# Optimization experiments

Hardware: AMD Instinct MI355X
Metric: run time of the kernel (lower is better)

Reference implementation:

```python
import jax, jax.numpy as jnp
import numpy as np

HEADS = 8
DIM_HEAD = 64
CHUNK = 128
EPS = 1e-6
KERNEL_EPS = 1e-4


def softmax_kernel(x, proj, is_query):
    # x: [b,h,n,d], proj: [f,d]  (FAVOR+ positive softmax features)
    d = x.shape[-1]
    data_normalizer = d ** -0.25
    ratio = proj.shape[0] ** -0.5
    data_dash = jnp.einsum('bhnd,fd->bhnf', x * data_normalizer, proj)
    diag = 0.5 * (data_normalizer ** 2) * jnp.sum(x * x, axis=-1, keepdims=True)  # [b,h,n,1]
    if is_query:
        m = jnp.max(data_dash, axis=-1, keepdims=True)
    else:
        m = jnp.max(data_dash, axis=(-1, -2), keepdims=True)
    return ratio * (jnp.exp(data_dash - diag - jax.lax.stop_gradient(m)) + KERNEL_EPS)


def infer_hidden_states(q, k, v, chunk_size=CHUNK):
    # q,k: [b,h,n,f], v: [b,h,n,e]; chunked causal linear attention with carried cumsums
    b, h, n, f = q.shape
    e = v.shape[-1]
    nc = n // chunk_size

    def to_chunks(t):
        return jnp.moveaxis(t.reshape(b, h, nc, chunk_size, t.shape[-1]), 2, 0)

    qs, ks, vs = to_chunks(q), to_chunks(k), to_chunks(v)

    def step(carry, inp):
        Z, S = carry  # [b,h,1,f], [b,h,1,f,e]
        qc, kc, vc = inp
        k_cum = Z + jnp.cumsum(kc, axis=2)                       # [b,h,c,f]
        D_inv = 1.0 / jnp.einsum('bhnf,bhnf->bhn', qc, k_cum + EPS)
        ctx = jnp.einsum('bhnf,bhne->bhnfe', kc, vc)             # [b,h,c,f,e]
        ctx_cum = S + jnp.cumsum(ctx, axis=2)
        out = jnp.einsum('bhnfe,bhnf,bhn->bhne', ctx_cum, qc, D_inv)
        return (k_cum[:, :, -1:], ctx_cum[:, :, -1:]), out

    init = (jnp.zeros((b, h, 1, f), q.dtype), jnp.zeros((b, h, 1, f, e), q.dtype))
    (Z, S), outs = jax.lax.scan(step, init, (qs, ks, vs))
    out = jnp.moveaxis(outs, 0, 2).reshape(b, h, n, e)
    return out, Z[:, :, 0], S[:, :, 0]


def reference(x, proj, Wq, Wk, Wv, Wo, bo):
    b, n, dim = x.shape
    h, dh = HEADS, DIM_HEAD

    def split_heads(t):
        return jnp.transpose(t.reshape(b, n, h, dh), (0, 2, 1, 3))

    q = split_heads(x @ Wq)
    k = split_heads(x @ Wk)
    v = split_heads(x @ Wv)

    qf = softmax_kernel(q, proj, is_query=True)
    kf = softmax_kernel(k, proj, is_query=False)

    out, Z, S = infer_hidden_states(qf, kf, v)
    out = jnp.transpose(out, (0, 2, 1, 3)).reshape(b, n, h * dh)
    out = out @ Wo + bo
    return out, Z, S


def setup_inputs() -> dict:
    key = jax.random.key(0)
    ks = jax.random.split(key, 6)
    b, n, dim = 2, 2048, 512
    f = 256
    return {
        'x': jax.random.normal(ks[0], (b, n, dim), jnp.float32),
        'proj': jax.random.normal(ks[1], (f, DIM_HEAD), jnp.float32),
        'Wq': jax.random.normal(ks[2], (dim, dim), jnp.float32) * (dim ** -0.5),
        'Wk': jax.random.normal(ks[3], (dim, dim), jnp.float32) * (dim ** -0.5),
        'Wv': jax.random.normal(ks[4], (dim, dim), jnp.float32) * (dim ** -0.5),
        'Wo': jax.random.normal(ks[5], (dim, dim), jnp.float32) * (dim ** -0.5),
        'bo': jnp.zeros((dim,), jnp.float32),
    }
```

## Files before the change

kernel.cpp:

```cpp
#include <hip/hip_runtime.h>
#include <hip/hip_bf16.h>
#include <math.h>

#define NB    2
#define NSEQ  2048
#define DIMM  512
#define NH    8
#define DHd   64
#define FF    256
#define CHK   128
#define NCHK  16
#define NBH   16

typedef unsigned short ushort_t;
typedef __attribute__((ext_vector_type(8))) __bf16 bf16x8;
typedef __attribute__((ext_vector_type(4))) float floatx4;

__device__ __forceinline__ unsigned short f2bf(float x) {
    union { __hip_bfloat16 h; unsigned short u; } v;
    v.h = __float2bfloat16(x);
    return v.u;
}
__device__ __forceinline__ float bf2f(unsigned short u) {
    union { unsigned short u2[2]; float f; } v;
    v.u2[0] = 0; v.u2[1] = u;
    return v.f;
}
__device__ __forceinline__ unsigned enc_f(float x) {
    unsigned u = __float_as_uint(x);
    return (u & 0x80000000u) ? ~u : (u | 0x80000000u);
}
__device__ __forceinline__ float dec_f(unsigned e) {
    unsigned u = (e & 0x80000000u) ? (e & 0x7fffffffu) : ~e;
    return __uint_as_float(u);
}

__device__ __forceinline__ void gload16(const void* g, void* l) {
    __builtin_amdgcn_global_load_lds(
        (const __attribute__((address_space(1))) void*)g,
        (__attribute__((address_space(3))) void*)l, 16, 0, 0);
}

__device__ __forceinline__ bf16x8 frag8(const ushort_t* lds, int row, int kb) {
    return *((const bf16x8*)lds + row * 8 + (kb ^ (row & 7)));
}
__device__ __forceinline__ bf16x8 fragS(const ushort_t* lds, int row, int kb) {
    return *((const bf16x8*)lds + row * 16 + (kb ^ (row & 15)));
}

__global__ __launch_bounds__(256)
void prep(const float* __restrict__ x, const float* __restrict__ proj,
          const float* __restrict__ W0, const float* __restrict__ W1,
          const float* __restrict__ W2, const float* __restrict__ W3,
          ushort_t* __restrict__ xb, ushort_t* __restrict__ projb,
          ushort_t* __restrict__ T0, ushort_t* __restrict__ T1,
          ushort_t* __restrict__ T2, ushort_t* __restrict__ T3,
          unsigned* __restrict__ mk_u)
{
    __shared__ float t[32][33];
    const int b = blockIdx.x, tid = threadIdx.x;
    if (b < 2048) {
        const int gid = b * 256 + tid;
        const float4 v = *(const float4*)(x + (size_t)gid * 4);
        union { ushort4 v4; unsigned short s[4]; } pk;
        pk.s[0] = f2bf(v.x); pk.s[1] = f2bf(v.y); pk.s[2] = f2bf(v.z); pk.s[3] = f2bf(v.w);
        ((ushort4*)xb)[gid] = pk.v4;
    } else if (b < 2064) {
        const int gid = (b - 2048) * 256 + tid;
        const float dn = 0.35355339059327379f;
        const float4 v = *(const float4*)(proj + (size_t)gid * 4);
        union { ushort4 v4; unsigned short s[4]; } pk;
        pk.s[0] = f2bf(v.x * dn); pk.s[1] = f2bf(v.y * dn);
        pk.s[2] = f2bf(v.z * dn); pk.s[3] = f2bf(v.w * dn);
        ((ushort4*)projb)[gid] = pk.v4;
    } else if (b < 3088) {
        const int idx = b - 2064;
        const int z = idx >> 8, rem = idx & 255;
        const int bx = rem & 15, by = rem >> 4;
        const float* W = (z == 0) ? W0 : (z == 1) ? W1 : (z == 2) ? W2 : W3;
        ushort_t* T = (z == 0) ? T0 : (z == 1) ? T1 : (z == 2) ? T2 : T3;
        const int x0 = bx * 32, y0 = by * 32;
        const int tx = tid & 31, ty = tid >> 5;
#pragma unroll
        for (int i = 0; i < 4; i++)
            t[ty + i * 8][tx] = W[(size_t)(y0 + ty + i * 8) * DIMM + x0 + tx];
        __syncthreads();
#pragma unroll
        for (int i = 0; i < 4; i++)
            T[(size_t)(x0 + ty + i * 8) * DIMM + y0 + tx] = f2bf(t[tx][ty + i * 8]);
    } else {
        if (tid < NBH) mk_u[tid] = 0u;
    }
}

__device__ __forceinline__ void mfma_mainloop(
    const ushort_t* __restrict__ AG, const ushort_t* __restrict__ BG,
    ushort_t* As, ushort_t* Bs, int ldA, int ldB, int K,
    floatx4 acc[4][4], int tid)
{
    const int lane = tid & 63, wid = tid >> 6;
    const int q = lane >> 4, c = lane & 15;
    const int wm = (wid >> 1) * 64, wn = (wid & 1) * 64;

    for (int k0 = 0; k0 < K; k0 += 64) {
#pragma unroll
        for (int t = 0; t < 4; t++) {
            const int g = t * 256 + tid, r = g >> 3, kb = (g & 7) ^ (r & 7);
            gload16(AG + (size_t)r * ldA + k0 + kb * 8, As + (size_t)g * 8);
        }
#pragma unroll
        for (int t = 0; t < 4; t++) {
            const int g = t * 256 + tid, r = g >> 3, kb = (g & 7) ^ (r & 7);
            gload16(BG + (size_t)r * ldB + k0 + kb * 8, Bs + (size_t)g * 8);
        }
        __syncthreads();
#pragma unroll
        for (int ks = 0; ks < 2; ks++) {
            bf16x8 af[4], bfr[4];
#pragma unroll
            for (int i = 0; i < 4; i++) {
                af[i]  = frag8(As, wm + i * 16 + c, ks * 4 + q);
                bfr[i] = frag8(Bs, wn + i * 16 + c, ks * 4 + q);
            }
#pragma unroll
            for (int i = 0; i < 4; i++)
#pragma unroll
                for (int j = 0; j < 4; j++)
                    acc[i][j] = __builtin_amdgcn_mfma_f32_16x16x32_bf16(
                        af[i], bfr[j], acc[i][j], 0, 0, 0);
        }
        __syncthreads();
    }
}

__global__ __launch_bounds__(256)
void gemm_qkv(const ushort_t* __restrict__ xb,
              const ushort_t* __restrict__ Wtq, const ushort_t* __restrict__ Wtk,
              const ushort_t* __restrict__ Wtv, const ushort_t* __restrict__ projb,
              ushort_t* __restrict__ qb, ushort_t* __restrict__ kb,
              ushort_t* __restrict__ vTb, unsigned* __restrict__ mk_u)
{
    __shared__ alignas(16) ushort_t SM[25600];
    __shared__ float red[256];
    ushort_t* As = SM;
    ushort_t* Bs = SM + 8192;
    ushort_t* PS = SM + 17408;
    const int tid = threadIdx.x;
    const int n0 = blockIdx.x * 128, m0 = blockIdx.y * 128, z = blockIdx.z;
    const ushort_t* Bt = (z == 0) ? Wtq : ((z == 1) ? Wtk : Wtv);

    floatx4 zero = {0.f, 0.f, 0.f, 0.f};
    floatx4 acc[4][4];
#pragma unroll
    for (int i = 0; i < 4; i++)
#pragma unroll
        for (int j = 0; j < 4; j++) acc[i][j] = zero;

    mfma_mainloop(xb + (size_t)m0 * DIMM, Bt + (size_t)n0 * DIMM, As, Bs,
                  DIMM, DIMM, DIMM, acc, tid);

    const int lane = tid & 63, wid = tid >> 6;
    const int q = lane >> 4, cl = lane & 15;
    const int wm = (wid >> 1) * 64, wn = (wid & 1) * 64;

#pragma unroll
    for (int i = 0; i < 4; i++)
#pragma unroll
        for (int j = 0; j < 4; j++) {
            const int col = wn + j * 16 + cl;
#pragma unroll
            for (int r = 0; r < 4; r++) {
                const int row = wm + i * 16 + q * 4 + r;
                SM[row * 136 + col] = f2bf(acc[i][j][r]);
            }
        }
    __syncthreads();

    if (z < 2) {
        ushort_t* ob = (z == 0) ? qb : kb;
        if (z == 1) {
#pragma unroll
            for (int t = 0; t < 4; t++) {
                const int g = t * 256 + tid, f = g >> 3, kbg = (g & 7) ^ (f & 7);
                gload16(projb + (size_t)f * 64 + kbg * 8, PS + (size_t)g * 8);
            }
        }
#pragma unroll
        for (int p = 0; p < 16; p++) {
            const int idx = p * 256 + tid;
            const int row = idx >> 5, c4 = idx & 31;
            ushort4 o = *(const ushort4*)&SM[row * 136 + c4 * 4];
            *(ushort4*)(ob + (size_t)(m0 + row) * DIMM + n0 + c4 * 4) = o;
        }
        if (z == 1) {
            const int bb = m0 >> 11;
            const int h0 = n0 >> 6;
            float mx[2] = {-3.0e38f, -3.0e38f};
#pragma unroll
            for (int half = 0; half < 2; half++) {
                __syncthreads();
#pragma unroll
                for (int hh = 0; hh < 2; hh++) {
                    floatx4 a2[4][4];
#pragma unroll
                    for (int i = 0; i < 4; i++)
#pragma unroll
                        for (int j = 0; j < 4; j++) a2[i][j] = zero;
#pragma unroll
                    for (int ks = 0; ks < 2; ks++) {
                        bf16x8 af[4], bfr[4];
#pragma unroll
                        for (int i = 0; i < 4; i++)
                            af[i] = *(const bf16x8*)&SM[(wm + i * 16 + cl) * 136 + hh * 64 + (ks * 4 + q) * 8];
#pragma unroll
                        for (int j = 0; j < 4; j++)
                            bfr[j] = frag8(PS, wn + j * 16 + cl, ks * 4 + q);
#pragma unroll
                        for (int i = 0; i < 4; i++)
#pragma unroll
                            for (int j = 0; j < 4; j++)
                                a2[i][j] = __builtin_amdgcn_mfma_f32_16x16x32_bf16(
                                    af[i], bfr[j], a2[i][j], 0, 0, 0);
                    }
#pragma unroll
                    for (int i = 0; i < 4; i++)
#pragma unroll
                        for (int j = 0; j < 4; j++)
#pragma unroll
                            for (int r = 0; r < 4; r++) mx[hh] = fmaxf(mx[hh], a2[i][j][r]);
                }
                if (half == 0) {
                    __syncthreads();
#pragma unroll
                    for (int t = 0; t < 4; t++) {
                        const int g = t * 256 + tid, f = g >> 3, kbg = (g & 7) ^ (f & 7);
                        gload16(projb + (size_t)(128 + f) * 64 + kbg * 8, PS + (size_t)g * 8);
                    }
                }
            }
#pragma unroll
            for (int hh = 0; hh < 2; hh++) {
                __syncthreads();
                red[tid] = mx[hh];
                __syncthreads();
                for (int s = 128; s > 0; s >>= 1) {
                    if (tid < s) red[tid] = fmaxf(red[tid], red[tid + s]);
                    __syncthreads();
                }
                if (tid == 0) atomicMax(&mk_u[bb * NH + h0 + hh], enc_f(red[0]));
            }
        }
    } else {
        const int bb = m0 >> 11, nbase = m0 & 2047;
#pragma unroll
        for (int p = 0; p < 16; p++) {
            const int idx = p * 256 + tid;
            const int cl2 = idx >> 5, n4 = idx & 31;
            const int C = n0 + cl2;
            const int h = C >> 6, e = C & 63;
            union { ushort4 v4; unsigned short s[4]; } pk;
#pragma unroll
            for (int k = 0; k < 4; k++) pk.s[k] = SM[(n4 * 4 + k) * 136 + cl2];
            *(ushort4*)(vTb + (((size_t)(bb * NH + h) * 64 + e)) * NSEQ + nbase + n4 * 4) = pk.v4;
        }
    }
}

__global__ __launch_bounds__(256)
void gemm_out(const ushort_t* __restrict__ attnb, const ushort_t* __restrict__ Wto,
              float* __restrict__ out, const float* __restrict__ bias)
{
    __shared__ alignas(16) ushort_t As[8192];
    __shared__ alignas(16) ushort_t Bs[8192];
    const int tid = threadIdx.x;
    const int n0 = blockIdx.x * 128, m0 = blockIdx.y * 128;

    floatx4 zero = {0.f, 0.f, 0.f, 0.f};
    floatx4 acc[4][4];
#pragma unroll
    for (int i = 0; i < 4; i++)
#pragma unroll
        for (int j = 0; j < 4; j++) acc[i][j] = zero;

    mfma_mainloop(attnb + (size_t)m0 * DIMM, Wto + (size_t)n0 * DIMM, As, Bs,
                  DIMM, DIMM, DIMM, acc, tid);

    const int lane = tid & 63, wid = tid >> 6;
    const int q = lane >> 4, c = lane & 15;
    const int wm = (wid >> 1) * 64, wn = (wid & 1) * 64;
#pragma unroll
    for (int i = 0; i < 4; i++)
#pragma unroll
        for (int j = 0; j < 4; j++) {
            const int col = n0 + wn + j * 16 + c;
            const float bv = bias[col];
#pragma unroll
            for (int r = 0; r < 4; r++) {
                const int row = m0 + wm + i * 16 + q * 4 + r;
                out[(size_t)row * DIMM + col] = acc[i][j][r] + bv;
            }
        }
}

__global__ __launch_bounds__(256)
void featk(const ushort_t* __restrict__ kb_, const ushort_t* __restrict__ projb,
           const unsigned* __restrict__ mk_u, const ushort_t* __restrict__ vTb,
           ushort_t* __restrict__ kfb, float* __restrict__ CTXT,
           float* __restrict__ Ksum)
{
    __shared__ alignas(16) ushort_t SM[24576];
    __shared__ float dtmp[256];
    __shared__ float diag_l[128];
    __shared__ float colp[2][256];
    ushort_t* As = SM;
    ushort_t* Bs = SM + 8192;
    const int tid = threadIdx.x, lane = tid & 63, wid = tid >> 6;
    const int q = lane >> 4, cl = lane & 15;
    const int m0 = blockIdx.x * 128, h = blockIdx.y;
    const int bb = m0 >> 11, nloc = m0 & 2047;
    const int bh = bb * NH + h;
    const int cidx = nloc >> 7;
    const ushort_t* Aq = kb_ + (size_t)m0 * DIMM + h * 64;

    {
        const int row = tid >> 1, half = tid & 1;
        float s = 0.f;
        const ushort_t* p = Aq + (size_t)row * DIMM + half * 32;
#pragma unroll
        for (int d = 0; d < 32; d += 4) {
            ushort4 w = *(const ushort4*)(p + d);
            float a = bf2f(w.x), b2 = bf2f(w.y), c2 = bf2f(w.z), d2 = bf2f(w.w);
            s += a * a + b2 * b2 + c2 * c2 + d2 * d2;
        }
        dtmp[tid] = s;
    }
    __syncthreads();
    if (tid < 128) diag_l[tid] = (dtmp[2 * tid] + dtmp[2 * tid + 1]) * 0.0625f;

#pragma unroll
    for (int t = 0; t < 4; t++) {
        const int g = t * 256 + tid, r = g >> 3, kb = (g & 7) ^ (r & 7);
        gload16(Aq + (size_t)r * DIMM + kb * 8, As + (size_t)g * 8);
    }
#pragma unroll
    for (int t = 0; t < 8; t++) {
        const int g = t * 256 + tid, r = g >> 3, kb = (g & 7) ^ (r & 7);
        gload16(projb + (size_t)r * 64 + kb * 8, Bs + (size_t)g * 8);
    }
    __syncthreads();

    floatx4 zero = {0.f, 0.f, 0.f, 0.f};
    floatx4 acc[4][8];
#pragma unroll
    for (int i = 0; i < 4; i++)
#pragma unroll
        for (int j = 0; j < 8; j++) acc[i][j] = zero;
    const int wm = (wid >> 1) * 64, wn = (wid & 1) * 128;
#pragma unroll
    for (int ks = 0; ks < 2; ks++) {
        bf16x8 af[4], bfr[8];
#pragma unroll
        for (int i = 0; i < 4; i++) af[i] = frag8(As, wm + i * 16 + cl, ks * 4 + q);
#pragma unroll
        for (int j = 0; j < 8; j++) bfr[j] = frag8(Bs, wn + j * 16 + cl, ks * 4 + q);
#pragma unroll
        for (int i = 0; i < 4; i++)
#pragma unroll
            for (int j = 0; j < 8; j++)
                acc[i][j] = __builtin_amdgcn_mfma_f32_16x16x32_bf16(
                    af[i], bfr[j], acc[i][j], 0, 0, 0);
    }
    __syncthreads();

    const float mk = dec_f(mk_u[bh]);
#pragma unroll
    for (int i = 0; i < 4; i++)
#pragma unroll
        for (int r = 0; r < 4; r++) {
            const int row = wm + i * 16 + q * 4 + r;
            const float cc = diag_l[row] + mk;
#pragma unroll
            for (int j = 0; j < 8; j++)
                acc[i][j][r] = 0.0625f * (__expf(acc[i][j][r] - cc) + 1.0e-4f);
        }

#pragma unroll
    for (int j = 0; j < 8; j++) {
        float s = 0.f;
#pragma unroll
        for (int i = 0; i < 4; i++)
            s += acc[i][j][0] + acc[i][j][1] + acc[i][j][2] + acc[i][j][3];
        s += __shfl_xor(s, 16);
        s += __shfl_xor(s, 32);
        if (q == 0) colp[wid >> 1][wn + j * 16 + cl] = s;
    }

    const size_t frow = (size_t)bh * NSEQ + nloc;
#pragma unroll
    for (int hf = 0; hf < 2; hf++) {
        __syncthreads();
        if ((wid & 1) == hf) {
#pragma unroll
            for (int i = 0; i < 4; i++)
#pragma unroll
                for (int j = 0; j < 8; j++) {
                    const int col = j * 16 + cl;
#pragma unroll
                    for (int r = 0; r < 4; r++) {
                        const int row = wm + i * 16 + q * 4 + r;
                        SM[row * 132 + col] = f2bf(acc[i][j][r]);
                    }
                }
        }
        if (hf == 0) {
            Ksum[((size_t)bh * NCHK + cidx) * FF + tid] = colp[0][tid] + colp[1][tid];
        }
        __syncthreads();
#pragma unroll
        for (int p = 0; p < 16; p++) {
            const int idx = p * 256 + tid;
            const int row = idx >> 5, c4 = idx & 31;
            ushort4 o = *(const ushort4*)&SM[row * 132 + c4 * 4];
            *(ushort4*)(kfb + (frow + row) * FF + hf * 128 + c4 * 4) = o;
        }
    }

    __syncthreads();
    ushort_t* Vs = SM;
    ushort_t* T  = SM + 8192;
    const ushort_t* Vg = vTb + ((size_t)bh * 64) * NSEQ + nloc;
#pragma unroll
    for (int t = 0; t < 4; t++) {
        const int g = t * 256 + tid, r = g >> 4, kb = (g & 15) ^ (r & 15);
        gload16(Vg + (size_t)r * NSEQ + kb * 8, Vs + (size_t)g * 8);
    }

    const size_t cbase = ((size_t)bh * NCHK + cidx) * 64;
#pragma unroll
    for (int fq = 0; fq < 4; fq++) {
        if ((wid & 1) == (fq >> 1)) {
#pragma unroll
            for (int jj = 0; jj < 4; jj++) {
                const int j = (fq & 1) * 4 + jj;
#pragma unroll
                for (int i = 0; i < 4; i++)
#pragma unroll
                    for (int r = 0; r < 4; r++) {
                        const int n = wm + i * 16 + q * 4 + r;
                        T[(jj * 16 + cl) * 136 + n] = f2bf(acc[i][j][r]);
                    }
            }
        }
        __syncthreads();
        floatx4 accc[4];
#pragma unroll
        for (int jj = 0; jj < 4; jj++) accc[jj] = zero;
#pragma unroll
        for (int kt = 0; kt < 4; kt++) {
            const bf16x8 av = fragS(Vs, wid * 16 + cl, kt * 4 + q);
#pragma unroll
            for (int jj = 0; jj < 4; jj++) {
                const bf16x8 bv = *(const bf16x8*)(T + (jj * 16 + cl) * 136 + (kt * 4 + q) * 8);
                accc[jj] = __builtin_amdgcn_mfma_f32_16x16x32_bf16(av, bv, accc[jj], 0, 0, 0);
            }
        }
#pragma unroll
        for (int jj = 0; jj < 4; jj++) {
            const int f = fq * 64 + jj * 16 + cl;
#pragma unroll
            for (int r = 0; r < 4; r++) {
                const int e = wid * 16 + q * 4 + r;
                CTXT[(cbase + e) * FF + f] = accc[jj][r];
            }
        }
        __syncthreads();
    }
}

__global__ void prefix_zs(float* __restrict__ Ksum, float* __restrict__ Zout,
                          const float* __restrict__ CTXT, ushort_t* __restrict__ ctxp,
                          float* __restrict__ Sout)
{
    const int b = blockIdx.x;
    if (b < 1024) {
        const int idx = b * 256 + threadIdx.x;
        const int bh = idx >> 14, ef = idx & 16383;
        const int e = ef >> 8, f = ef & 255;
        float run = 0.f;
#pragma unroll
        for (int c = 0; c < NCHK; c++) {
            const size_t o = (((size_t)bh * NCHK + c) * 64 + e) * FF + f;
            const float t = CTXT[o];
            ctxp[o] = f2bf(run);
            run += t;
        }
        Sout[((size_t)bh * FF + f) * 64 + e] = run;
    } else {
        const int idx = (b - 1024) * 256 + threadIdx.x;
        const int bh = idx >> 8, f = idx & 255;
        float run = 0.f;
#pragma unroll
        for (int c = 0; c < NCHK; c++) {
            const size_t o = ((size_t)(bh * NCHK + c)) * FF + f;
            const float t = Ksum[o];
            Ksum[o] = run;
            run += t;
        }
        Zout[(size_t)bh * FF + f] = run;
    }
}

__global__ __launch_bounds__(256)
void chunk_out_mfma(const ushort_t* __restrict__ qb_, const ushort_t* __restrict__ projb,
                    const ushort_t* __restrict__ kfb, const ushort_t* __restrict__ vTb,
                    const float* __restrict__ Zex, const ushort_t* __restrict__ ctxp,
                    ushort_t* __restrict__ attnb)
{
    __shared__ alignas(16) ushort_t QF[32768];
    __shared__ alignas(16) ushort_t Sld[16384];
    __shared__ alignas(16) ushort_t As[8192];
    __shared__ alignas(16) ushort_t Bs[8192];
    __shared__ float zeps[256];
    __shared__ float rows_part[2][128];
    __shared__ float denp[256];
    __shared__ float den_l[128];
    __shared__ float dtmp[256];
    __shared__ float diag_l[128];
    __shared__ float mx2[2][128];

    const int tid = threadIdx.x, lane = tid & 63, wid = tid >> 6;
    const int q = lane >> 4, cl = lane & 15;
    const int bh = blockIdx.x >> 4, c = blockIdx.x & 15;
    const int bb = bh >> 3, h = bh & 7;
    const int n0 = c * CHK;
    const ushort_t* Kf = kfb + ((size_t)bh * NSEQ + n0) * FF;
    const ushort_t* Aq = qb_ + ((size_t)(bb * NSEQ + n0)) * DIMM + h * 64;

    zeps[tid] = Zex[((size_t)bh * NCHK + c) * FF + tid] + 1.0e-6f;

    {
        const int row = tid >> 1, half = tid & 1;
        float s = 0.f;
        const ushort_t* p = Aq + (size_t)row * DIMM + half * 32;
#pragma unroll
        for (int d = 0; d < 32; d += 4) {
            ushort4 w = *(const ushort4*)(p + d);
            float a = bf2f(w.x), b2 = bf2f(w.y), c2 = bf2f(w.z), d2 = bf2f(w.w);
            s += a * a + b2 * b2 + c2 * c2 + d2 * d2;
        }
        dtmp[tid] = s;
    }
    __syncthreads();
    if (tid < 128) diag_l[tid] = (dtmp[2 * tid] + dtmp[2 * tid + 1]) * 0.0625f;

#pragma unroll
    for (int t = 0; t < 4; t++) {
        const int g = t * 256 + tid, r = g >> 3, kb = (g & 7) ^ (r & 7);
        gload16(Aq + (size_t)r * DIMM + kb * 8, As + (size_t)g * 8);
    }
#pragma unroll
    for (int t = 0; t < 8; t++) {
        const int g = t * 256 + tid, r = g >> 3, kb = (g & 7) ^ (r & 7);
        gload16(projb + (size_t)r * 64 + kb * 8, Sld + (size_t)g * 8);
    }
    __syncthreads();

    floatx4 zero = {0.f, 0.f, 0.f, 0.f};
    {
        floatx4 accq[4][8];
#pragma unroll
        for (int i = 0; i < 4; i++)
#pragma unroll
            for (int j = 0; j < 8; j++) accq[i][j] = zero;
        const int wmF = (wid >> 1) * 64, wnF = (wid & 1) * 128;
#pragma unroll
        for (int ks = 0; ks < 2; ks++) {
            bf16x8 af[4], bfr[8];
#pragma unroll
            for (int i = 0; i < 4; i++) af[i] = frag8(As, wmF + i * 16 + cl, ks * 4 + q);
#pragma unroll
            for (int j = 0; j < 8; j++) bfr[j] = frag8(Sld, wnF + j * 16 + cl, ks * 4 + q);
#pragma unroll
            for (int i = 0; i < 4; i++)
#pragma unroll
                for (int j = 0; j < 8; j++)
                    accq[i][j] = __builtin_amdgcn_mfma_f32_16x16x32_bf16(
                        af[i], bfr[j], accq[i][j], 0, 0, 0);
        }
#pragma unroll
        for (int i = 0; i < 4; i++)
#pragma unroll
            for (int r = 0; r < 4; r++) {
                const int row = wmF + i * 16 + q * 4 + r;
                float mx = -3.0e38f;
#pragma unroll
                for (int j = 0; j < 8; j++) mx = fmaxf(mx, accq[i][j][r]);
                mx = fmaxf(mx, __shfl_xor(mx, 1)); mx = fmaxf(mx, __shfl_xor(mx, 2));
                mx = fmaxf(mx, __shfl_xor(mx, 4)); mx = fmaxf(mx, __shfl_xor(mx, 8));
                if (cl == 0) mx2[wid & 1][row] = mx;
            }
        __syncthreads();
#pragma unroll
        for (int i = 0; i < 4; i++)
#pragma unroll
            for (int r = 0; r < 4; r++) {
                const int row = wmF + i * 16 + q * 4 + r;
                const float cc = diag_l[row] + fmaxf(mx2[0][row], mx2[1][row]);
#pragma unroll
                for (int j = 0; j < 8; j++) {
                    const int col = wnF + j * 16 + cl;
                    const float v = 0.0625f * (__expf(accq[i][j][r] - cc) + 1.0e-4f);
                    const int s = col >> 6, fp = col & 63;
                    QF[s * 8192 + (row * 8 + ((fp >> 3) ^ (row & 7))) * 8 + (fp & 7)] = f2bf(v);
                }
            }
    }
    __syncthreads();

    floatx4 acc1[4][4];
#pragma unroll
    for (int i = 0; i < 4; i++)
#pragma unroll
        for (int j = 0; j < 4; j++) acc1[i][j] = zero;
    const int wm = (wid >> 1) * 64, wn = (wid & 1) * 64;
    for (int k0 = 0; k0 < FF; k0 += 64) {
#pragma unroll
        for (int t = 0; t < 4; t++) {
            const int g = t * 256 + tid, r = g >> 3, kb = (g & 7) ^ (r & 7);
            gload16(Kf + (size_t)r * FF + k0 + kb * 8, Bs + (size_t)g * 8);
        }
        __syncthreads();
        const ushort_t* QFs = QF + (k0 >> 6) * 8192;
#pragma unroll
        for (int ks = 0; ks < 2; ks++) {
            bf16x8 af[4], bfr[4];
#pragma unroll
            for (int i = 0; i < 4; i++) {
                af[i]  = frag8(QFs, wm + i * 16 + cl, ks * 4 + q);
                bfr[i] = frag8(Bs, wn + i * 16 + cl, ks * 4 + q);
            }
#pragma unroll
            for (int i = 0; i < 4; i++)
#pragma unroll
                for (int j = 0; j < 4; j++)
                    acc1[i][j] = __builtin_amdgcn_mfma_f32_16x16x32_bf16(
                        af[i], bfr[j], acc1[i][j], 0, 0, 0);
        }
        __syncthreads();
    }
#pragma unroll
    for (int i = 0; i < 4; i++)
#pragma unroll
        for (int r = 0; r < 4; r++) {
            const int row = wm + i * 16 + q * 4 + r;
            float part = 0.f;
#pragma unroll
            for (int j = 0; j < 4; j++) {
                const int col = wn + j * 16 + cl;
                const float v = (col <= row) ? acc1[i][j][r] : 0.f;
                part += v;
                Sld[(row * 16 + ((col >> 3) ^ (row & 15))) * 8 + (col & 7)] = f2bf(v);
            }
            part += __shfl_xor(part, 1); part += __shfl_xor(part, 2);
            part += __shfl_xor(part, 4); part += __shfl_xor(part, 8);
            if (cl == 0) rows_part[wid & 1][row] = part;
        }
    __syncthreads();

    floatx4 acc2[4][2];
#pragma unroll
    for (int i = 0; i < 4; i++)
#pragma unroll
        for (int j = 0; j < 2; j++) acc2[i][j] = zero;
    const ushort_t* Vt = vTb + ((size_t)bh * 64) * NSEQ + n0;
    for (int k0 = 0; k0 < CHK; k0 += 64) {
#pragma unroll
        for (int t = 0; t < 2; t++) {
            const int g = t * 256 + tid, r = g >> 3, kb = (g & 7) ^ (r & 7);
            gload16(Vt + (size_t)r * NSEQ + k0 + kb * 8, As + (size_t)g * 8);
        }
        __syncthreads();
#pragma unroll
        for (int ks = 0; ks < 2; ks++) {
            bf16x8 af[4], bfr[2];
            const int kbS = (k0 >> 3) + ks * 4 + q;
#pragma unroll
            for (int i = 0; i < 4; i++) af[i] = frag8(As, i * 16 + cl, ks * 4 + q);
#pragma unroll
            for (int j = 0; j < 2; j++) bfr[j] = fragS(Sld, wid * 32 + j * 16 + cl, kbS);
#pragma unroll
            for (int i = 0; i < 4; i++)
#pragma unroll
                for (int j = 0; j < 2; j++)
                    acc2[i][j] = __builtin_amdgcn_mfma_f32_16x16x32_bf16(
                        af[i], bfr[j], acc2[i][j], 0, 0, 0);
        }
        __syncthreads();
    }

    const ushort_t* Cp = ctxp + ((size_t)bh * NCHK + c) * 64 * FF;
    float dacc = 0.f;
    const int drow = tid & 127, dhalf = tid >> 7;
    for (int k0 = 0; k0 < FF; k0 += 64) {
#pragma unroll
        for (int t = 0; t < 2; t++) {
            const int g = t * 256 + tid, r = g >> 3, kb = (g & 7) ^ (r & 7);
            gload16(Cp + (size_t)r * FF + k0 + kb * 8, As + (size_t)g * 8);
        }
        __syncthreads();
        const ushort_t* QFs = QF + (k0 >> 6) * 8192;
#pragma unroll
        for (int ks = 0; ks < 2; ks++) {
            bf16x8 af[4], bfr[2];
#pragma unroll
            for (int i = 0; i < 4; i++) af[i] = frag8(As, i * 16 + cl, ks * 4 + q);
#pragma unroll
            for (int j = 0; j < 2; j++) bfr[j] = frag8(QFs, wid * 32 + j * 16 + cl, ks * 4 + q);
#pragma unroll
            for (int i = 0; i < 4; i++)
#pragma unroll
                for (int j = 0; j < 2; j++)
                    acc2[i][j] = __builtin_amdgcn_mfma_f32_16x16x32_bf16(
                        af[i], bfr[j], acc2[i][j], 0, 0, 0);
        }
#pragma unroll
        for (int gi = 0; gi < 4; gi++) {
            const int kb = dhalf * 4 + gi;
            const ushort_t* gp = QFs + ((size_t)drow * 8 + (kb ^ (drow & 7))) * 8;
            const int kbase = k0 + kb * 8;
#pragma unroll
            for (int e2 = 0; e2 < 8; e2++)
                dacc = fmaf(bf2f(gp[e2]), zeps[kbase + e2], dacc);
        }
        __syncthreads();
    }
    denp[tid] = dacc;
    __syncthreads();
    if (tid < 128)
        den_l[tid] = rows_part[0][tid] + rows_part[1][tid] + denp[tid] + denp[tid + 128];
    __syncthreads();

#pragma unroll
    for (int j = 0; j < 2; j++) {
        const int row = wid * 32 + j * 16 + cl;
        const float dinv = 1.0f / den_l[row];
#pragma unroll
        for (int i = 0; i < 4; i++)
#pragma unroll
            for (int r = 0; r < 4; r++) {
                const int e = i * 16 + q * 4 + r;
                Sld[row * 68 + e] = f2bf(acc2[i][j][r] * dinv);
            }
    }
    __syncthreads();
#pragma unroll
    for (int p = 0; p < 8; p++) {
        const int idx = p * 256 + tid;
        const int row = idx >> 4, e4 = idx & 15;
        ushort4 o = *(const ushort4*)&Sld[row * 68 + e4 * 4];
        *(ushort4*)(attnb + ((size_t)(bb * NSEQ + n0 + row)) * DIMM + h * 64 + e4 * 4) = o;
    }
}

extern "C" void kernel_launch(void* const* d_in, const int* in_sizes, int n_in,
                              void* d_out, int out_size, void* d_ws, size_t ws_size,
                              hipStream_t stream)
{
    (void)in_sizes; (void)n_in; (void)out_size; (void)ws_size;
    const float* x    = (const float*)d_in[0];
    const float* proj = (const float*)d_in[1];
    const float* Wq   = (const float*)d_in[2];
    const float* Wk   = (const float*)d_in[3];
    const float* Wv   = (const float*)d_in[4];
    const float* Wo   = (const float*)d_in[5];
    const float* bo   = (const float*)d_in[6];
    float* out = (float*)d_out;

    char* W = (char*)d_ws;
    float*    CTXT = (float*)W;              W += (size_t)16777216;
    ushort_t* kfb  = (ushort_t*)W;           W += (size_t)16777216;
    ushort_t* ctxp = (ushort_t*)W;           W += (size_t)8388608;
    ushort_t* qb   = (ushort_t*)W;           W += (size_t)4194304;
    ushort_t* kb   = (ushort_t*)W;           W += (size_t)4194304;
    ushort_t* xb   = (ushort_t*)W;           W += (size_t)4194304;
    ushort_t* vTb  = (ushort_t*)W;           W += (size_t)4194304;
    ushort_t* Wtq  = (ushort_t*)W;           W += (size_t)524288;
    ushort_t* Wtk  = (ushort_t*)W;           W += (size_t)524288;
    ushort_t* Wtv  = (ushort_t*)W;           W += (size_t)524288;
    ushort_t* Wto  = (ushort_t*)W;           W += (size_t)524288;
    ushort_t* projb = (ushort_t*)W;          W += (size_t)32768;
    float*    Ksum = (float*)W;              W += (size_t)262144;
    unsigned* mk_u = (unsigned*)W;           W += (size_t)256;

    ushort_t* attnb = xb;

    float* Zout = out + (size_t)4096 * 512;
    float* Sout = Zout + (size_t)NBH * FF;

    hipLaunchKernelGGL(prep, dim3(3089), dim3(256), 0, stream,
                       x, proj, Wq, Wk, Wv, Wo, xb, projb, Wtq, Wtk, Wtv, Wto, mk_u);
    hipLaunchKernelGGL(gemm_qkv, dim3(4, 32, 3), dim3(256), 0, stream,
                       xb, Wtq, Wtk, Wtv, projb, qb, kb, vTb, mk_u);
    hipLaunchKernelGGL(featk, dim3(32, 8), dim3(256), 0, stream,
                       kb, projb, mk_u, vTb, kfb, CTXT, Ksum);
    hipLaunchKernelGGL(prefix_zs, dim3(1040), dim3(256), 0, stream,
                       Ksum, Zout, CTXT, ctxp, Sout);
    hipLaunchKernelGGL(chunk_out_mfma, dim3(256), dim3(256), 0, stream,
                       qb, projb, kfb, vTb, Ksum, ctxp, attnb);
    hipLaunchKernelGGL(gemm_out, dim3(4, 32), dim3(256), 0, stream, attnb, Wto, out, bo);
}
```

Baseline: 148.3 us.

## Double-buffer GEMM mainloops, prefetch operands early, and halve gemm_out M-tile

Reworks the shared GEMM mainloop into a double-buffered LDS pipeline, so the next K-slice is loaded while MFMAs run on the current one, and removes one barrier per step. In featk and chunk_out_mfma, V, Kf and ctx tiles are prefetched into spare LDS regions earlier, which collapses several load/sync/compute loops into straight-line MFMA sequences. gemm_out now uses 64-row tiles and twice as many blocks to fill the CUs better. The cost is more LDS per block, which may lower occupancy, and the buffer reuse across phases is fragile.

New measurement: 177.3 us. 1.2x slower.

```diff
diff --git a/kernel.cpp b/kernel.cpp
--- a/kernel.cpp
+++ b/kernel.cpp
@@ -46,6 +46,61 @@
 }
 __device__ __forceinline__ bf16x8 fragS(const ushort_t* lds, int row, int kb) {
     return *((const bf16x8*)lds + row * 16 + (kb ^ (row & 15)));
+}
+
+__device__ __forceinline__ void stage8(const ushort_t* __restrict__ G, ushort_t* dst,
+                                       int ld, int tid) {
+#pragma unroll
+    for (int t = 0; t < 4; t++) {
+        const int g = t * 256 + tid, r = g >> 3, kb = (g & 7) ^ (r & 7);
+        gload16(G + (size_t)r * ld + kb * 8, dst + (size_t)g * 8);
+    }
+}
+__device__ __forceinline__ void stage4h(const ushort_t* __restrict__ G, ushort_t* dst,
+                                        int ld, int tid) {
+#pragma unroll
+    for (int t = 0; t < 2; t++) {
+        const int g = t * 256 + tid, r = g >> 3, kb = (g & 7) ^ (r & 7);
+        gload16(G + (size_t)r * ld + kb * 8, dst + (size_t)g * 8);
+    }
+}
+
+__device__ __forceinline__ void mm_step44(const ushort_t* A, const ushort_t* B,
+                                          floatx4 acc[4][4], int wm, int wn, int cl, int q)
+{
+#pragma unroll
+    for (int ks = 0; ks < 2; ks++) {
+        bf16x8 af[4], bfr[4];
+#pragma unroll
+        for (int i = 0; i < 4; i++) {
+            af[i]  = frag8(A, wm + i * 16 + cl, ks * 4 + q);
+            bfr[i] = frag8(B, wn + i * 16 + cl, ks * 4 + q);
+        }
+#pragma unroll
+        for (int i = 0; i < 4; i++)
+#pragma unroll
+            for (int j = 0; j < 4; j++)
+                acc[i][j] = __builtin_amdgcn_mfma_f32_16x16x32_bf16(
+                    af[i], bfr[j], acc[i][j], 0, 0, 0);
+    }
+}
+__device__ __forceinline__ void mm_step24(const ushort_t* A, const ushort_t* B,
+                                          floatx4 acc[2][4], int wm, int wn, int cl, int q)
+{
+#pragma unroll
+    for (int ks = 0; ks < 2; ks++) {
+        bf16x8 af[2], bfr[4];
+#pragma unroll
+        for (int i = 0; i < 2; i++) af[i] = frag8(A, wm + i * 16 + cl, ks * 4 + q);
+#pragma unroll
+        for (int j = 0; j < 4; j++) bfr[j] = frag8(B, wn + j * 16 + cl, ks * 4 + q);
+#pragma unroll
+        for (int i = 0; i < 2; i++)
+#pragma unroll
+            for (int j = 0; j < 4; j++)
+                acc[i][j] = __builtin_amdgcn_mfma_f32_16x16x32_bf16(
+                    af[i], bfr[j], acc[i][j], 0, 0, 0);
+    }
 }
 
 __global__ __launch_bounds__(256)
@@ -95,40 +150,30 @@
 
 __device__ __forceinline__ void mfma_mainloop(
     const ushort_t* __restrict__ AG, const ushort_t* __restrict__ BG,
-    ushort_t* As, ushort_t* Bs, int ldA, int ldB, int K,
-    floatx4 acc[4][4], int tid)
+    ushort_t* SM, int ldA, int ldB, floatx4 acc[4][4], int tid)
 {
     const int lane = tid & 63, wid = tid >> 6;
     const int q = lane >> 4, c = lane & 15;
     const int wm = (wid >> 1) * 64, wn = (wid & 1) * 64;
-
-    for (int k0 = 0; k0 < K; k0 += 64) {
-#pragma unroll
-        for (int t = 0; t < 4; t++) {
-            const int g = t * 256 + tid, r = g >> 3, kb = (g & 7) ^ (r & 7);
-            gload16(AG + (size_t)r * ldA + k0 + kb * 8, As + (size_t)g * 8);
-        }
-#pragma unroll
-        for (int t = 0; t < 4; t++) {
-            const int g = t * 256 + tid, r = g >> 3, kb = (g & 7) ^ (r & 7);
-            gload16(BG + (size_t)r * ldB + k0 + kb * 8, Bs + (size_t)g * 8);
-        }
-        __syncthreads();
-#pragma unroll
-        for (int ks = 0; ks < 2; ks++) {
-            bf16x8 af[4], bfr[4];
-#pragma unroll
-            for (int i = 0; i < 4; i++) {
-                af[i]  = frag8(As, wm + i * 16 + c, ks * 4 + q);
-                bfr[i] = frag8(Bs, wn + i * 16 + c, ks * 4 + q);
-            }
-#pragma unroll
-            for (int i = 0; i < 4; i++)
-#pragma unroll
-                for (int j = 0; j < 4; j++)
-                    acc[i][j] = __builtin_amdgcn_mfma_f32_16x16x32_bf16(
-                        af[i], bfr[j], acc[i][j], 0, 0, 0);
-        }
+    ushort_t* A0 = SM;
+    ushort_t* B0 = SM + 8192;
+    ushort_t* A1 = SM + 16384;
+    ushort_t* B1 = SM + 24576;
+
+    stage8(AG, A0, ldA, tid);
+    stage8(BG, B0, ldB, tid);
+    __syncthreads();
+    for (int tt = 0; tt < 4; tt++) {
+        const int k0 = tt * 128;
+        stage8(AG + k0 + 64, A1, ldA, tid);
+        stage8(BG + k0 + 64, B1, ldB, tid);
+        mm_step44(A0, B0, acc, wm, wn, c, q);
+        __syncthreads();
+        if (tt < 3) {
+            stage8(AG + k0 + 128, A0, ldA, tid);
+            stage8(BG + k0 + 128, B0, ldB, tid);
+        }
+        mm_step44(A1, B1, acc, wm, wn, c, q);
         __syncthreads();
     }
 }
@@ -140,10 +185,8 @@
               ushort_t* __restrict__ qb, ushort_t* __restrict__ kb,
               ushort_t* __restrict__ vTb, unsigned* __restrict__ mk_u)
 {
-    __shared__ alignas(16) ushort_t SM[25600];
+    __shared__ alignas(16) ushort_t SM[32768];
     __shared__ float red[256];
-    ushort_t* As = SM;
-    ushort_t* Bs = SM + 8192;
     ushort_t* PS = SM + 17408;
     const int tid = threadIdx.x;
     const int n0 = blockIdx.x * 128, m0 = blockIdx.y * 128, z = blockIdx.z;
@@ -156,8 +199,8 @@
 #pragma unroll
         for (int j = 0; j < 4; j++) acc[i][j] = zero;
 
-    mfma_mainloop(xb + (size_t)m0 * DIMM, Bt + (size_t)n0 * DIMM, As, Bs,
-                  DIMM, DIMM, DIMM, acc, tid);
+    mfma_mainloop(xb + (size_t)m0 * DIMM, Bt + (size_t)n0 * DIMM, SM,
+                  DIMM, DIMM, acc, tid);
 
     const int lane = tid & 63, wid = tid >> 6;
     const int q = lane >> 4, cl = lane & 15;
@@ -270,26 +313,46 @@
 void gemm_out(const ushort_t* __restrict__ attnb, const ushort_t* __restrict__ Wto,
               float* __restrict__ out, const float* __restrict__ bias)
 {
-    __shared__ alignas(16) ushort_t As[8192];
-    __shared__ alignas(16) ushort_t Bs[8192];
+    __shared__ alignas(16) ushort_t SM[24576];
+    ushort_t* A0 = SM;
+    ushort_t* A1 = SM + 4096;
+    ushort_t* B0 = SM + 8192;
+    ushort_t* B1 = SM + 16384;
     const int tid = threadIdx.x;
-    const int n0 = blockIdx.x * 128, m0 = blockIdx.y * 128;
+    const int n0 = blockIdx.x * 128, m0 = blockIdx.y * 64;
+    const ushort_t* AG = attnb + (size_t)m0 * DIMM;
+    const ushort_t* BG = Wto + (size_t)n0 * DIMM;
 
     floatx4 zero = {0.f, 0.f, 0.f, 0.f};
-    floatx4 acc[4][4];
-#pragma unroll
-    for (int i = 0; i < 4; i++)
+    floatx4 acc[2][4];
+#pragma unroll
+    for (int i = 0; i < 2; i++)
 #pragma unroll
         for (int j = 0; j < 4; j++) acc[i][j] = zero;
-
-    mfma_mainloop(attnb + (size_t)m0 * DIMM, Wto + (size_t)n0 * DIMM, As, Bs,
-                  DIMM, DIMM, DIMM, acc, tid);
 
     const int lane = tid & 63, wid = tid >> 6;
     const int q = lane >> 4, c = lane & 15;
-    const int wm = (wid >> 1) * 64, wn = (wid & 1) * 64;
-#pragma unroll
-    for (int i = 0; i < 4; i++)
+    const int wm = (wid >> 1) * 32, wn = (wid & 1) * 64;
+
+    stage4h(AG, A0, DIMM, tid);
+    stage8(BG, B0, DIMM, tid);
+    __syncthreads();
+    for (int tt = 0; tt < 4; tt++) {
+        const int k0 = tt * 128;
+        stage4h(AG + k0 + 64, A1, DIMM, tid);
+        stage8(BG + k0 + 64, B1, DIMM, tid);
+        mm_step24(A0, B0, acc, wm, wn, c, q);
+        __syncthreads();
+        if (tt < 3) {
+            stage4h(AG + k0 + 128, A0, DIMM, tid);
+            stage8(BG + k0 + 128, B0, DIMM, tid);
+        }
+        mm_step24(A1, B1, acc, wm, wn, c, q);
+        __syncthreads();
+    }
+
+#pragma unroll
+    for (int i = 0; i < 2; i++)
 #pragma unroll
         for (int j = 0; j < 4; j++) {
             const int col = n0 + wn + j * 16 + c;
@@ -308,12 +371,13 @@
            ushort_t* __restrict__ kfb, float* __restrict__ CTXT,
            float* __restrict__ Ksum)
 {
-    __shared__ alignas(16) ushort_t SM[24576];
+    __shared__ alignas(16) ushort_t SM[32768];
     __shared__ float dtmp[256];
     __shared__ float diag_l[128];
     __shared__ float colp[2][256];
     ushort_t* As = SM;
     ushort_t* Bs = SM + 8192;
+    ushort_t* Vs = SM + 24576;
     const int tid = threadIdx.x, lane = tid & 63, wid = tid >> 6;
     const int q = lane >> 4, cl = lane & 15;
     const int m0 = blockIdx.x * 128, h = blockIdx.y;
@@ -321,6 +385,7 @@
     const int bh = bb * NH + h;
     const int cidx = nloc >> 7;
     const ushort_t* Aq = kb_ + (size_t)m0 * DIMM + h * 64;
+    const ushort_t* Vg = vTb + ((size_t)bh * 64) * NSEQ + nloc;
 
     {
         const int row = tid >> 1, half = tid & 1;
@@ -346,6 +411,11 @@
     for (int t = 0; t < 8; t++) {
         const int g = t * 256 + tid, r = g >> 3, kb = (g & 7) ^ (r & 7);
         gload16(projb + (size_t)r * 64 + kb * 8, Bs + (size_t)g * 8);
+    }
+#pragma unroll
+    for (int t = 0; t < 4; t++) {
+        const int g = t * 256 + tid, r = g >> 4, kb = (g & 15) ^ (r & 15);
+        gload16(Vg + (size_t)r * NSEQ + kb * 8, Vs + (size_t)g * 8);
     }
     __syncthreads();
 
@@ -426,14 +496,7 @@
     }
 
     __syncthreads();
-    ushort_t* Vs = SM;
-    ushort_t* T  = SM + 8192;
-    const ushort_t* Vg = vTb + ((size_t)bh * 64) * NSEQ + nloc;
-#pragma unroll
-    for (int t = 0; t < 4; t++) {
-        const int g = t * 256 + tid, r = g >> 4, kb = (g & 15) ^ (r & 15);
-        gload16(Vg + (size_t)r * NSEQ + kb * 8, Vs + (size_t)g * 8);
-    }
+    ushort_t* T = SM + 8192;
 
     const size_t cbase = ((size_t)bh * NCHK + cidx) * 64;
 #pragma unroll
@@ -507,6 +570,36 @@
             run += t;
         }
         Zout[(size_t)bh * FF + f] = run;
+    }
+}
+
+__device__ __forceinline__ void pv_step(const ushort_t* Cb, const ushort_t* QFs,
+                                        floatx4 acc2[4][2], float& dacc,
+                                        const float* zeps, int kglob,
+                                        int wid, int cl, int q, int drow, int dhalf)
+{
+#pragma unroll
+    for (int ks = 0; ks < 2; ks++) {
+        bf16x8 af[4], bfr[2];
+#pragma unroll
+        for (int i = 0; i < 4; i++) af[i] = frag8(Cb, i * 16 + cl, ks * 4 + q);
+#pragma unroll
+        for (int j = 0; j < 2; j++) bfr[j] = frag8(QFs, wid * 32 + j * 16 + cl, ks * 4 + q);
+#pragma unroll
+        for (int i = 0; i < 4; i++)
+#pragma unroll
+            for (int j = 0; j < 2; j++)
+                acc2[i][j] = __builtin_amdgcn_mfma_f32_16x16x32_bf16(
+                    af[i], bfr[j], acc2[i][j], 0, 0, 0);
+    }
+#pragma unroll
+    for (int gi = 0; gi < 4; gi++) {
+        const int kb = dhalf * 4 + gi;
+        const ushort_t* gp = QFs + ((size_t)drow * 8 + (kb ^ (drow & 7))) * 8;
+        const int kbase = kglob + kb * 8;
+#pragma unroll
+        for (int e2 = 0; e2 < 8; e2++)
+            dacc = fmaf(bf2f(gp[e2]), zeps[kbase + e2], dacc);
     }
 }
 
@@ -553,16 +646,13 @@
     __syncthreads();
     if (tid < 128) diag_l[tid] = (dtmp[2 * tid] + dtmp[2 * tid + 1]) * 0.0625f;
 
-#pragma unroll
-    for (int t = 0; t < 4; t++) {
-        const int g = t * 256 + tid, r = g >> 3, kb = (g & 7) ^ (r & 7);
-        gload16(Aq + (size_t)r * DIMM + kb * 8, As + (size_t)g * 8);
-    }
+    stage8(Aq, As, DIMM, tid);
 #pragma unroll
     for (int t = 0; t < 8; t++) {
         const int g = t * 256 + tid, r = g >> 3, kb = (g & 7) ^ (r & 7);
         gload16(projb + (size_t)r * 64 + kb * 8, Sld + (size_t)g * 8);
     }
+    stage8(Kf, Bs, FF, tid);
     __syncthreads();
 
     floatx4 zero = {0.f, 0.f, 0.f, 0.f};
@@ -600,6 +690,11 @@
                 if (cl == 0) mx2[wid & 1][row] = mx;
             }
         __syncthreads();
+
+        stage8(Kf + 64,  As, FF, tid);
+        stage8(Kf + 128, Sld, FF, tid);
+        stage8(Kf + 192, Sld + 8192, FF, tid);
+
 #pragma unroll
         for (int i = 0; i < 4; i++)
 #pragma unroll
@@ -623,31 +718,20 @@
 #pragma unroll
         for (int j = 0; j < 4; j++) acc1[i][j] = zero;
     const int wm = (wid >> 1) * 64, wn = (wid & 1) * 64;
-    for (int k0 = 0; k0 < FF; k0 += 64) {
-#pragma unroll
-        for (int t = 0; t < 4; t++) {
-            const int g = t * 256 + tid, r = g >> 3, kb = (g & 7) ^ (r & 7);
-            gload16(Kf + (size_t)r * FF + k0 + kb * 8, Bs + (size_t)g * 8);
-        }
-        __syncthreads();
-        const ushort_t* QFs = QF + (k0 >> 6) * 8192;
-#pragma unroll
-        for (int ks = 0; ks < 2; ks++) {
-            bf16x8 af[4], bfr[4];
-#pragma unroll
-            for (int i = 0; i < 4; i++) {
-                af[i]  = frag8(QFs, wm + i * 16 + cl, ks * 4 + q);
-                bfr[i] = frag8(Bs, wn + i * 16 + cl, ks * 4 + q);
-            }
-#pragma unroll
-            for (int i = 0; i < 4; i++)
-#pragma unroll
-                for (int j = 0; j < 4; j++)
-                    acc1[i][j] = __builtin_amdgcn_mfma_f32_16x16x32_bf16(
-                        af[i], bfr[j], acc1[i][j], 0, 0, 0);
-        }
-        __syncthreads();
-    }
+#pragma unroll
+    for (int kt = 0; kt < 4; kt++) {
+        const ushort_t* Tb = (kt == 0) ? Bs : (kt == 1) ? As : (kt == 2) ? Sld : (Sld + 8192);
+        mm_step44(QF + kt * 8192, Tb, acc1, wm, wn, cl, q);
+    }
+    __syncthreads();
+
+    const ushort_t* Vt = vTb + ((size_t)bh * 64) * NSEQ + n0;
+    const ushort_t* Cp = ctxp + ((size_t)bh * NCHK + c) * 64 * FF;
+    stage4h(Vt, Bs, NSEQ, tid);
+    stage4h(Vt + 64, Bs + 4096, NSEQ, tid);
+    stage4h(Cp, As, FF, tid);
+    stage4h(Cp + 64, As + 4096, FF, tid);
+
 #pragma unroll
     for (int i = 0; i < 4; i++)
 #pragma unroll
@@ -672,22 +756,16 @@
     for (int i = 0; i < 4; i++)
 #pragma unroll
         for (int j = 0; j < 2; j++) acc2[i][j] = zero;
-    const ushort_t* Vt = vTb + ((size_t)bh * 64) * NSEQ + n0;
-    for (int k0 = 0; k0 < CHK; k0 += 64) {
-#pragma unroll
-        for (int t = 0; t < 2; t++) {
-            const int g = t * 256 + tid, r = g >> 3, kb = (g & 7) ^ (r & 7);
-            gload16(Vt + (size_t)r * NSEQ + k0 + kb * 8, As + (size_t)g * 8);
-        }
-        __syncthreads();
+#pragma unroll
+    for (int kt = 0; kt < 2; kt++) {
+        const ushort_t* Vtb = kt ? (Bs + 4096) : Bs;
 #pragma unroll
         for (int ks = 0; ks < 2; ks++) {
             bf16x8 af[4], bfr[2];
-            const int kbS = (k0 >> 3) + ks * 4 + q;
-#pragma unroll
-            for (int i = 0; i < 4; i++) af[i] = frag8(As, i * 16 + cl, ks * 4 + q);
-#pragma unroll
-            for (int j = 0; j < 2; j++) bfr[j] = fragS(Sld, wid * 32 + j * 16 + cl, kbS);
+#pragma unroll
+            for (int i = 0; i < 4; i++) af[i] = frag8(Vtb, i * 16 + cl, ks * 4 + q);
+#pragma unroll
+            for (int j = 0; j < 2; j++) bfr[j] = fragS(Sld, wid * 32 + j * 16 + cl, kt * 8 + ks * 4 + q);
 #pragma unroll
             for (int i = 0; i < 4; i++)
 #pragma unroll
@@ -695,45 +773,20 @@
                     acc2[i][j] = __builtin_amdgcn_mfma_f32_16x16x32_bf16(
                         af[i], bfr[j], acc2[i][j], 0, 0, 0);
         }
-        __syncthreads();
-    }
-
-    const ushort_t* Cp = ctxp + ((size_t)bh * NCHK + c) * 64 * FF;
+    }
+    __syncthreads();
+
+    stage4h(Cp + 128, Bs, FF, tid);
+    stage4h(Cp + 192, Bs + 4096, FF, tid);
+
     float dacc = 0.f;
     const int drow = tid & 127, dhalf = tid >> 7;
-    for (int k0 = 0; k0 < FF; k0 += 64) {
-#pragma unroll
-        for (int t = 0; t < 2; t++) {
-            const int g = t * 256 + tid, r = g >> 3, kb = (g & 7) ^ (r & 7);
-            gload16(Cp + (size_t)r * FF + k0 + kb * 8, As + (size_t)g * 8);
-        }
-        __syncthreads();
-        const ushort_t* QFs = QF + (k0 >> 6) * 8192;
-#pragma unroll
-        for (int ks = 0; ks < 2; ks++) {
-            bf16x8 af[4], bfr[2];
-#pragma unroll
-            for (int i = 0; i < 4; i++) af[i] = frag8(As, i * 16 + cl, ks * 4 + q);
-#pragma unroll
-            for (int j = 0; j < 2; j++) bfr[j] = frag8(QFs, wid * 32 + j * 16 + cl, ks * 4 + q);
-#pragma unroll
-            for (int i = 0; i < 4; i++)
-#pragma unroll
-                for (int j = 0; j < 2; j++)
-                    acc2[i][j] = __builtin_amdgcn_mfma_f32_16x16x32_bf16(
-                        af[i], bfr[j], acc2[i][j], 0, 0, 0);
-        }
-#pragma unroll
-        for (int gi = 0; gi < 4; gi++) {
-            const int kb = dhalf * 4 + gi;
-            const ushort_t* gp = QFs + ((size_t)drow * 8 + (kb ^ (drow & 7))) * 8;
-            const int kbase = k0 + kb * 8;
-#pragma unroll
-            for (int e2 = 0; e2 < 8; e2++)
-                dacc = fmaf(bf2f(gp[e2]), zeps[kbase + e2], dacc);
-        }
-        __syncthreads();
-    }
+    pv_step(As,        QF,         acc2, dacc, zeps, 0,   wid, cl, q, drow, dhalf);
+    pv_step(As + 4096, QF + 8192,  acc2, dacc, zeps, 64,  wid, cl, q, drow, dhalf);
+    __syncthreads();
+    pv_step(Bs,        QF + 16384, acc2, dacc, zeps, 128, wid, cl, q, drow, dhalf);
+    pv_step(Bs + 4096, QF + 24576, acc2, dacc, zeps, 192, wid, cl, q, drow, dhalf);
+
     denp[tid] = dacc;
     __syncthreads();
     if (tid < 128)
@@ -807,5 +860,5 @@
                        Ksum, Zout, CTXT, ctxp, Sout);
     hipLaunchKernelGGL(chunk_out_mfma, dim3(256), dim3(256), 0, stream,
                        qb, projb, kfb, vTb, Ksum, ctxp, attnb);
-    hipLaunchKernelGGL(gemm_out, dim3(4, 32), dim3(256), 0, stream, attnb, Wto, out, bo);
-}
+    hipLaunchKernelGGL(gemm_out, dim3(4, 64), dim3(256), 0, stream, attnb, Wto, out, bo);
+}
```
